# Kernel tuning notes

Hardware: AMD Instinct MI355X
Metric: run time of the kernel (lower is better)

## Reference

```python
import jax, jax.numpy as jnp
import numpy as np

D_MODEL = 256
N_HEADS = 4
D_HEAD = D_MODEL // N_HEADS
SCALE = 1.0 / np.sqrt(D_HEAD).astype(np.float32)


def setup_inputs() -> dict:
    key = jax.random.key(0)
    ks = jax.random.split(key, 8)
    B, T, S = 4, 512, 512
    return {
        "query": jax.random.normal(ks[0], (B, T, D_MODEL), dtype=jnp.float32),
        "key": jax.random.normal(ks[1], (B, S, D_MODEL), dtype=jnp.float32),
        "value": jax.random.normal(ks[2], (B, S, D_MODEL), dtype=jnp.float32),
        "w_q": jax.random.normal(ks[3], (D_MODEL, D_MODEL), dtype=jnp.float32) * 0.05,
        "w_k": jax.random.normal(ks[4], (D_MODEL, D_MODEL), dtype=jnp.float32) * 0.05,
        "w_v": jax.random.normal(ks[5], (D_MODEL, D_MODEL), dtype=jnp.float32) * 0.05,
        "v_a": jax.random.normal(ks[6], (N_HEADS, D_HEAD), dtype=jnp.float32),
        "w_o": jax.random.normal(ks[7], (D_MODEL, D_MODEL), dtype=jnp.float32) * 0.05,
    }


def reference(query, key, value, w_q, w_k, w_v, v_a, w_o):
    B, T, _ = query.shape
    S = key.shape[1]
    # projections; weights stored as (out, in) like nn.Linear -> x @ W.T
    Q = (query @ w_q.T).reshape(B, T, N_HEADS, D_HEAD).transpose(0, 2, 1, 3)  # bhtd
    K = (key @ w_k.T).reshape(B, S, N_HEADS, D_HEAD).transpose(0, 2, 1, 3)    # bhsd
    V = (value @ w_v.T).reshape(B, S, N_HEADS, D_HEAD).transpose(0, 2, 1, 3)  # bhsd
    # additive (Bahdanau) scores: tanh broadcast of shape (B,H,T,S,Dh)
    combined = jnp.tanh(Q[:, :, :, None, :] + K[:, :, None, :, :])
    scores = jnp.einsum('bhtsd,hd->bhts', combined, v_a) * SCALE
    attn = jax.nn.softmax(scores, axis=-1)  # (B,H,T,S)
    attended = jnp.einsum('bhts,bhsd->bhtd', attn, V)
    attended = attended.transpose(0, 2, 1, 3).reshape(B, T, D_MODEL)
    out = attended @ w_o.T
    return out, attn
```

## Files before the change

kernel.cpp:

```cpp
#include <hip/hip_runtime.h>
#include <math.h>

#define BATCH 4
#define TLEN 512
#define SLEN 512
#define DM 256
#define NH 4
#define DH 64
#define BT (BATCH * TLEN)
#define WPAD 132

__device__ __forceinline__ float rcp_fast(float x) { return __builtin_amdgcn_rcpf(x); }

__device__ __forceinline__ void gemm_selfstage(const float* __restrict__ X,
                                               const float* __restrict__ W,
                                               float* __restrict__ wlds,
                                               int row0, int o0, int tid, int lane,
                                               float* acc) {
#pragma unroll
  for (int r = 0; r < 8; ++r) acc[r] = 0.f;
  const float* xb = X + (size_t)row0 * DM;
#pragma unroll 1
  for (int half = 0; half < 2; ++half) {
    __syncthreads();
    {
      const float4* wsrc = (const float4*)(W + (size_t)o0 * DM + half * 128);
#pragma unroll
      for (int i = 0; i < 8; ++i) {
        int c = i * 256 + tid;
        int row = c >> 5, kq = c & 31;
        *(float4*)&wlds[row * WPAD + kq * 4] = wsrc[(size_t)row * 64 + kq];
      }
    }
    __syncthreads();
    const float* xh = xb + half * 128;
#pragma unroll 2
    for (int kk = 0; kk < 128; kk += 4) {
      float4 w = *(const float4*)&wlds[lane * WPAD + kk];
#pragma unroll
      for (int r = 0; r < 8; ++r) {
        acc[r] = fmaf(xh[r * DM + kk + 0], w.x, acc[r]);
        acc[r] = fmaf(xh[r * DM + kk + 1], w.y, acc[r]);
        acc[r] = fmaf(xh[r * DM + kk + 2], w.z, acc[r]);
        acc[r] = fmaf(xh[r * DM + kk + 3], w.w, acc[r]);
      }
    }
  }
}

__global__ __launch_bounds__(256) void proj_kernel(
    const float* __restrict__ q, const float* __restrict__ k, const float* __restrict__ v,
    const float* __restrict__ wq, const float* __restrict__ wk, const float* __restrict__ wv,
    float* __restrict__ EQ, float* __restrict__ EKT, float* __restrict__ Vw) {
  __shared__ float wlds[64 * WPAD];
  int tid = threadIdx.x;
  int lane = tid & 63;
  int wid = __builtin_amdgcn_readfirstlane(tid >> 6);
  int which = blockIdx.y;
  const float* X = (which == 0) ? q : (which == 1) ? k : v;
  const float* W = (which == 0) ? wq : (which == 1) ? wk : wv;
  int row0 = (blockIdx.x >> 2) * 32 + wid * 8;
  int o0 = (blockIdx.x & 3) * 64;
  float acc[8];
  gemm_selfstage(X, W, wlds, row0, o0, tid, lane, acc);
  int o = o0 + lane;
  int h = o >> 6, d = o & 63;
#pragma unroll
  for (int r = 0; r < 8; ++r) {
    int row = row0 + r;
    int b = row >> 9, t = row & 511;
    int bh = b * NH + h;
    float val = acc[r];
    if (which < 2) {
      val = __expf(2.f * fminf(fmaxf(val, -5.5f), 5.5f));
    }
    if (which == 0) {
      EQ[((size_t)bh * TLEN + t) * DH + d] = val;
    } else if (which == 1) {
      EKT[(((size_t)bh * 16 + (d >> 2)) * SLEN + t) * 4 + (d & 3)] = val;
    } else {
      Vw[(size_t)bh * SLEN * DH + (size_t)(t >> 1) * 128 + d * 2 + (t & 1)] = val;
    }
  }
}

__global__ __launch_bounds__(256, 8) void attn_kernel(
    const float* __restrict__ EQ, const float* __restrict__ EKT,
    const float* __restrict__ Vw, const float* __restrict__ va_g,
    float* __restrict__ attn_out, float* __restrict__ attended) {
  __shared__ float pw[4][SLEN];
  __shared__ float fp[4][4][64];
  __shared__ float sred[4][4];
  int tid = threadIdx.x;
  int lane = tid & 63;
  int wid = __builtin_amdgcn_readfirstlane(tid >> 6);
  int bx = (int)((blockIdx.x & 7) * 256 + (blockIdx.x >> 3));
  int bh = bx >> 7;
  int tile = (bx & 127) * 4;
  int h = bh & 3, b = bh >> 2;
  int sq0 = wid * 128;

  const float4* ekf = (const float4*)EKT + (size_t)bh * (16 * SLEN) + sq0 + lane;
  const float* eqb = EQ + ((size_t)bh * TLEN + tile) * DH;
  const float* vap = va_g + h * DH;

  float acc[4][2];
#pragma unroll
  for (int t = 0; t < 4; ++t) { acc[t][0] = 0.f; acc[t][1] = 0.f; }
  float vsum = 0.f;

  float4 eA0, eA1, eB0, eB1;

#define LOADE(EV, dc_) do { EV##0 = ekf[(size_t)(dc_) * SLEN]; \
                            EV##1 = ekf[(size_t)(dc_) * SLEN + 64]; } while (0)

#define SC4(E, qv, av, aref) do {                                           \
    float A0 = fmaf(qv.x, E.x, 1.f), A1 = fmaf(qv.y, E.y, 1.f);             \
    float A2 = fmaf(qv.z, E.z, 1.f), A3 = fmaf(qv.w, E.w, 1.f);             \
    float n01 = fmaf(av.x, A1, av.y * A0);                                  \
    float n23 = fmaf(av.z, A3, av.w * A2);                                  \
    float P01 = A0 * A1, P23 = A2 * A3;                                     \
    float Nm = fmaf(n01, P23, n23 * P01);                                   \
    aref = fmaf(Nm, rcp_fast(P01 * P23), aref);                             \
  } while (0)

#define DCBODY(CUR, NXT, dc_) do {                                          \
    float4 av = *(const float4*)(vap + (dc_) * 4);                          \
    float4 q0 = *(const float4*)(eqb + 0 * DH + (dc_) * 4);                 \
    float4 q1 = *(const float4*)(eqb + 1 * DH + (dc_) * 4);                 \
    float4 q2 = *(const float4*)(eqb + 2 * DH + (dc_) * 4);                 \
    float4 q3 = *(const float4*)(eqb + 3 * DH + (dc_) * 4);                 \
    vsum += (av.x + av.y) + (av.z + av.w);                                  \
    if ((dc_) < 15) LOADE(NXT, (dc_) + 1);                                  \
    __builtin_amdgcn_sched_barrier(0);                                      \
    SC4(CUR##0, q0, av, acc[0][0]); SC4(CUR##1, q0, av, acc[0][1]);         \
    SC4(CUR##0, q1, av, acc[1][0]); SC4(CUR##1, q1, av, acc[1][1]);         \
    SC4(CUR##0, q2, av, acc[2][0]); SC4(CUR##1, q2, av, acc[2][1]);         \
    SC4(CUR##0, q3, av, acc[3][0]); SC4(CUR##1, q3, av, acc[3][1]);         \
  } while (0)

  LOADE(eA, 0);
#pragma unroll 1
  for (int dc2 = 0; dc2 < 8; ++dc2) {
    DCBODY(eA, eB, 2 * dc2);
    DCBODY(eB, eA, 2 * dc2 + 1);
  }

  size_t bht = (size_t)bh * TLEN + tile;
  float e0[4], e1[4];
#pragma unroll
  for (int t = 0; t < 4; ++t) {
    float x0 = __expf(fmaf(acc[t][0], -0.25f, vsum * 0.125f));
    float x1 = __expf(fmaf(acc[t][1], -0.25f, vsum * 0.125f));
    e0[t] = x0; e1[t] = x1;
    float es = x0 + x1;
#pragma unroll
    for (int off = 32; off; off >>= 1) es += __shfl_xor(es, off);
    if (lane == 0) sred[t][wid] = es;
  }
  __syncthreads();
#pragma unroll
  for (int t = 0; t < 4; ++t) {
    float es = (sred[t][0] + sred[t][1]) + (sred[t][2] + sred[t][3]);
    float inv = rcp_fast(es);
    float p0 = e0[t] * inv, p1 = e1[t] * inv;
    pw[t][sq0 + lane] = p0;
    pw[t][sq0 + 64 + lane] = p1;
    float* arow = attn_out + (bht + t) * SLEN + sq0;
    arow[lane] = p0;
    arow[64 + lane] = p1;
  }

  const float2* vb = (const float2*)Vw + (size_t)bh * (256 * 64) + (size_t)(wid * 64) * 64 + lane;
  float f[4];
#pragma unroll
  for (int t = 0; t < 4; ++t) f[t] = 0.f;
#pragma unroll 2
  for (int i = 0; i < 32; ++i) {
    float2 v01 = vb[(size_t)i * 128];
    float2 v23 = vb[(size_t)i * 128 + 64];
    int sb = sq0 + i * 4;
#pragma unroll
    for (int t = 0; t < 4; ++t) {
      float4 pq = *(const float4*)&pw[t][sb];
      f[t] = fmaf(pq.x, v01.x, f[t]);
      f[t] = fmaf(pq.y, v01.y, f[t]);
      f[t] = fmaf(pq.z, v23.x, f[t]);
      f[t] = fmaf(pq.w, v23.y, f[t]);
    }
  }
#pragma unroll
  for (int t = 0; t < 4; ++t) fp[wid][t][lane] = f[t];
  __syncthreads();
  {
    int t = wid;
    float s = (fp[0][t][lane] + fp[1][t][lane]) + (fp[2][t][lane] + fp[3][t][lane]);
    attended[((size_t)(b * TLEN) + tile + t) * DM + h * DH + lane] = s;
  }
}

__global__ __launch_bounds__(256) void outproj_kernel(
    const float* __restrict__ att, const float* __restrict__ wo,
    float* __restrict__ out) {
  __shared__ float wlds[64 * WPAD];
  int tid = threadIdx.x;
  int lane = tid & 63;
  int wid = __builtin_amdgcn_readfirstlane(tid >> 6);
  int row0 = (blockIdx.x >> 2) * 32 + wid * 8;
  int o0 = (blockIdx.x & 3) * 64;
  float acc[8];
  gemm_selfstage(att, wo, wlds, row0, o0, tid, lane, acc);
  int o = o0 + lane;
#pragma unroll
  for (int r = 0; r < 8; ++r)
    out[(size_t)(row0 + r) * DM + o] = acc[r];
}

extern "C" void kernel_launch(void* const* d_in, const int* in_sizes, int n_in,
                              void* d_out, int out_size, void* d_ws, size_t ws_size,
                              hipStream_t stream) {
  const float* query = (const float*)d_in[0];
  const float* key   = (const float*)d_in[1];
  const float* value = (const float*)d_in[2];
  const float* wq    = (const float*)d_in[3];
  const float* wk    = (const float*)d_in[4];
  const float* wv    = (const float*)d_in[5];
  const float* va    = (const float*)d_in[6];
  const float* wo    = (const float*)d_in[7];

  float* out  = (float*)d_out;
  float* attn = out + (size_t)BT * DM;

  const size_t SEG = (size_t)BT * DM;
  float* EQ  = (float*)d_ws;
  float* EKT = EQ + SEG;
  float* Vw  = EKT + SEG;
  float* att = Vw + SEG;

  proj_kernel<<<dim3(256, 3), 256, 0, stream>>>(query, key, value, wq, wk, wv, EQ, EKT, Vw);
  attn_kernel<<<dim3(2048), 256, 0, stream>>>(EQ, EKT, Vw, va, attn, att);
  outproj_kernel<<<dim3(256), 256, 0, stream>>>(att, wo, out);
}
```

Before: 101.8 us.

## Fuse projection, attention and output projection into one persistent kernel with grid barriers

Replaces the three separate launches with a single 1024-block persistent kernel. It has three phases: the QKV projection on 768 blocks, two attention tiles per block, and the output projection spread over 512 blocks with 4 rows per wave. The phases are separated by atomic-counter grid barriers. This removes inter-kernel launch gaps and tail effects, and swaps the padded weight staging in LDS for an XOR-swizzled layout. It relies on all 1024 blocks being co-resident. The barrier counters live in the last word of the att and out buffers, which later phases overwrite while some blocks may still be polling, so correctness depends on that timing.

```diff
diff --git a/kernel.cpp b/kernel.cpp
--- a/kernel.cpp
+++ b/kernel.cpp
@@ -8,112 +8,58 @@
 #define NH 4
 #define DH 64
 #define BT (BATCH * TLEN)
-#define WPAD 132
+#define NBLK 1024
 
 __device__ __forceinline__ float rcp_fast(float x) { return __builtin_amdgcn_rcpf(x); }
 
-__device__ __forceinline__ void gemm_selfstage(const float* __restrict__ X,
-                                               const float* __restrict__ W,
-                                               float* __restrict__ wlds,
-                                               int row0, int o0, int tid, int lane,
-                                               float* acc) {
-#pragma unroll
-  for (int r = 0; r < 8; ++r) acc[r] = 0.f;
-  const float* xb = X + (size_t)row0 * DM;
+__device__ __forceinline__ void grid_barrier(unsigned* ctr) {
+  __syncthreads();
+  if (threadIdx.x == 0) {
+    __threadfence();
+    __hip_atomic_fetch_add(ctr, 1u, __ATOMIC_RELAXED, __HIP_MEMORY_SCOPE_AGENT);
+    while (__hip_atomic_load(ctr, __ATOMIC_RELAXED, __HIP_MEMORY_SCOPE_AGENT) < NBLK)
+      __builtin_amdgcn_s_sleep(8);
+    __threadfence();
+  }
+  __syncthreads();
+}
+
+template <int RPT>
+__device__ __forceinline__ void panel_gemm(const float* __restrict__ X,
+                                           const float* __restrict__ W,
+                                           float* wl, int o0, int wrow0,
+                                           int tid, int lane, float* acc) {
+#pragma unroll
+  for (int r = 0; r < RPT; ++r) acc[r] = 0.f;
 #pragma unroll 1
   for (int half = 0; half < 2; ++half) {
     __syncthreads();
-    {
-      const float4* wsrc = (const float4*)(W + (size_t)o0 * DM + half * 128);
-#pragma unroll
-      for (int i = 0; i < 8; ++i) {
-        int c = i * 256 + tid;
-        int row = c >> 5, kq = c & 31;
-        *(float4*)&wlds[row * WPAD + kq * 4] = wsrc[(size_t)row * 64 + kq];
+    const float4* wsrc = (const float4*)(W + (size_t)o0 * DM + half * 128);
+#pragma unroll
+    for (int i = 0; i < 8; ++i) {
+      int c = i * 256 + tid;
+      int o = c >> 5, f = c & 31;
+      *(float4*)&wl[o * 128 + 4 * (f ^ (o & 7))] = wsrc[(size_t)o * 64 + f];
+    }
+    __syncthreads();
+    const float* xh = X + (size_t)wrow0 * DM + half * 128;
+#pragma unroll 4
+    for (int g = 0; g < 32; ++g) {
+      float4 w = *(const float4*)&wl[lane * 128 + 4 * (g ^ (lane & 7))];
+#pragma unroll
+      for (int r = 0; r < RPT; ++r) {
+        const float* xr = xh + r * DM + g * 4;
+        acc[r] = fmaf(xr[0], w.x, acc[r]);
+        acc[r] = fmaf(xr[1], w.y, acc[r]);
+        acc[r] = fmaf(xr[2], w.z, acc[r]);
+        acc[r] = fmaf(xr[3], w.w, acc[r]);
       }
     }
-    __syncthreads();
-    const float* xh = xb + half * 128;
-#pragma unroll 2
-    for (int kk = 0; kk < 128; kk += 4) {
-      float4 w = *(const float4*)&wlds[lane * WPAD + kk];
-#pragma unroll
-      for (int r = 0; r < 8; ++r) {
-        acc[r] = fmaf(xh[r * DM + kk + 0], w.x, acc[r]);
-        acc[r] = fmaf(xh[r * DM + kk + 1], w.y, acc[r]);
-        acc[r] = fmaf(xh[r * DM + kk + 2], w.z, acc[r]);
-        acc[r] = fmaf(xh[r * DM + kk + 3], w.w, acc[r]);
-      }
-    }
-  }
-}
-
-__global__ __launch_bounds__(256) void proj_kernel(
-    const float* __restrict__ q, const float* __restrict__ k, const float* __restrict__ v,
-    const float* __restrict__ wq, const float* __restrict__ wk, const float* __restrict__ wv,
-    float* __restrict__ EQ, float* __restrict__ EKT, float* __restrict__ Vw) {
-  __shared__ float wlds[64 * WPAD];
-  int tid = threadIdx.x;
-  int lane = tid & 63;
-  int wid = __builtin_amdgcn_readfirstlane(tid >> 6);
-  int which = blockIdx.y;
-  const float* X = (which == 0) ? q : (which == 1) ? k : v;
-  const float* W = (which == 0) ? wq : (which == 1) ? wk : wv;
-  int row0 = (blockIdx.x >> 2) * 32 + wid * 8;
-  int o0 = (blockIdx.x & 3) * 64;
-  float acc[8];
-  gemm_selfstage(X, W, wlds, row0, o0, tid, lane, acc);
-  int o = o0 + lane;
-  int h = o >> 6, d = o & 63;
-#pragma unroll
-  for (int r = 0; r < 8; ++r) {
-    int row = row0 + r;
-    int b = row >> 9, t = row & 511;
-    int bh = b * NH + h;
-    float val = acc[r];
-    if (which < 2) {
-      val = __expf(2.f * fminf(fmaxf(val, -5.5f), 5.5f));
-    }
-    if (which == 0) {
-      EQ[((size_t)bh * TLEN + t) * DH + d] = val;
-    } else if (which == 1) {
-      EKT[(((size_t)bh * 16 + (d >> 2)) * SLEN + t) * 4 + (d & 3)] = val;
-    } else {
-      Vw[(size_t)bh * SLEN * DH + (size_t)(t >> 1) * 128 + d * 2 + (t & 1)] = val;
-    }
-  }
-}
-
-__global__ __launch_bounds__(256, 8) void attn_kernel(
-    const float* __restrict__ EQ, const float* __restrict__ EKT,
-    const float* __restrict__ Vw, const float* __restrict__ va_g,
-    float* __restrict__ attn_out, float* __restrict__ attended) {
-  __shared__ float pw[4][SLEN];
-  __shared__ float fp[4][4][64];
-  __shared__ float sred[4][4];
-  int tid = threadIdx.x;
-  int lane = tid & 63;
-  int wid = __builtin_amdgcn_readfirstlane(tid >> 6);
-  int bx = (int)((blockIdx.x & 7) * 256 + (blockIdx.x >> 3));
-  int bh = bx >> 7;
-  int tile = (bx & 127) * 4;
-  int h = bh & 3, b = bh >> 2;
-  int sq0 = wid * 128;
-
-  const float4* ekf = (const float4*)EKT + (size_t)bh * (16 * SLEN) + sq0 + lane;
-  const float* eqb = EQ + ((size_t)bh * TLEN + tile) * DH;
-  const float* vap = va_g + h * DH;
-
-  float acc[4][2];
-#pragma unroll
-  for (int t = 0; t < 4; ++t) { acc[t][0] = 0.f; acc[t][1] = 0.f; }
-  float vsum = 0.f;
-
-  float4 eA0, eA1, eB0, eB1;
+  }
+}
 
 #define LOADE(EV, dc_) do { EV##0 = ekf[(size_t)(dc_) * SLEN]; \
                             EV##1 = ekf[(size_t)(dc_) * SLEN + 64]; } while (0)
-
 #define SC4(E, qv, av, aref) do {                                           \
     float A0 = fmaf(qv.x, E.x, 1.f), A1 = fmaf(qv.y, E.y, 1.f);             \
     float A2 = fmaf(qv.z, E.z, 1.f), A3 = fmaf(qv.w, E.w, 1.f);             \
@@ -123,7 +69,6 @@
     float Nm = fmaf(n01, P23, n23 * P01);                                   \
     aref = fmaf(Nm, rcp_fast(P01 * P23), aref);                             \
   } while (0)
-
 #define DCBODY(CUR, NXT, dc_) do {                                          \
     float4 av = *(const float4*)(vap + (dc_) * 4);                          \
     float4 q0 = *(const float4*)(eqb + 0 * DH + (dc_) * 4);                 \
@@ -139,6 +84,30 @@
     SC4(CUR##0, q3, av, acc[3][0]); SC4(CUR##1, q3, av, acc[3][1]);         \
   } while (0)
 
+__device__ __forceinline__ void attn_tile(int bxv,
+    const float* __restrict__ EQ, const float* __restrict__ EKT,
+    const float* __restrict__ Vw, const float* __restrict__ va_g,
+    float* __restrict__ attn_out, float* __restrict__ attended,
+    float* smem, int tid, int lane, int wid) {
+  float* pwf   = smem;
+  float* fpf   = smem + 2048;
+  float* sredf = smem + 3072;
+  int bx = (bxv & 7) * 256 + (bxv >> 3);
+  int bh = bx >> 7;
+  int tile = (bx & 127) * 4;
+  int h = bh & 3, b = bh >> 2;
+  int sq0 = wid * 128;
+
+  const float4* ekf = (const float4*)EKT + (size_t)bh * (16 * SLEN) + sq0 + lane;
+  const float* eqb = EQ + ((size_t)bh * TLEN + tile) * DH;
+  const float* vap = va_g + h * DH;
+
+  float acc[4][2];
+#pragma unroll
+  for (int t = 0; t < 4; ++t) { acc[t][0] = 0.f; acc[t][1] = 0.f; }
+  float vsum = 0.f;
+  float4 eA0, eA1, eB0, eB1;
+
   LOADE(eA, 0);
 #pragma unroll 1
   for (int dc2 = 0; dc2 < 8; ++dc2) {
@@ -156,16 +125,16 @@
     float es = x0 + x1;
 #pragma unroll
     for (int off = 32; off; off >>= 1) es += __shfl_xor(es, off);
-    if (lane == 0) sred[t][wid] = es;
+    if (lane == 0) sredf[t * 4 + wid] = es;
   }
   __syncthreads();
 #pragma unroll
   for (int t = 0; t < 4; ++t) {
-    float es = (sred[t][0] + sred[t][1]) + (sred[t][2] + sred[t][3]);
+    float es = (sredf[t * 4 + 0] + sredf[t * 4 + 1]) + (sredf[t * 4 + 2] + sredf[t * 4 + 3]);
     float inv = rcp_fast(es);
     float p0 = e0[t] * inv, p1 = e1[t] * inv;
-    pw[t][sq0 + lane] = p0;
-    pw[t][sq0 + 64 + lane] = p1;
+    pwf[t * SLEN + sq0 + lane] = p0;
+    pwf[t * SLEN + sq0 + 64 + lane] = p1;
     float* arow = attn_out + (bht + t) * SLEN + sq0;
     arow[lane] = p0;
     arow[64 + lane] = p1;
@@ -182,7 +151,7 @@
     int sb = sq0 + i * 4;
 #pragma unroll
     for (int t = 0; t < 4; ++t) {
-      float4 pq = *(const float4*)&pw[t][sb];
+      float4 pq = *(const float4*)&pwf[t * SLEN + sb];
       f[t] = fmaf(pq.x, v01.x, f[t]);
       f[t] = fmaf(pq.y, v01.y, f[t]);
       f[t] = fmaf(pq.z, v23.x, f[t]);
@@ -190,30 +159,73 @@
     }
   }
 #pragma unroll
-  for (int t = 0; t < 4; ++t) fp[wid][t][lane] = f[t];
+  for (int t = 0; t < 4; ++t) fpf[(wid * 4 + t) * 64 + lane] = f[t];
   __syncthreads();
   {
     int t = wid;
-    float s = (fp[0][t][lane] + fp[1][t][lane]) + (fp[2][t][lane] + fp[3][t][lane]);
+    float s = (fpf[(0 * 4 + t) * 64 + lane] + fpf[(1 * 4 + t) * 64 + lane]) +
+              (fpf[(2 * 4 + t) * 64 + lane] + fpf[(3 * 4 + t) * 64 + lane]);
     attended[((size_t)(b * TLEN) + tile + t) * DM + h * DH + lane] = s;
   }
 }
 
-__global__ __launch_bounds__(256) void outproj_kernel(
-    const float* __restrict__ att, const float* __restrict__ wo,
-    float* __restrict__ out) {
-  __shared__ float wlds[64 * WPAD];
+__global__ __launch_bounds__(256, 4) void fused_kernel(
+    const float* __restrict__ q, const float* __restrict__ k, const float* __restrict__ v,
+    const float* __restrict__ wq, const float* __restrict__ wk, const float* __restrict__ wv,
+    const float* __restrict__ va, const float* __restrict__ wo,
+    float* __restrict__ EQ, float* __restrict__ EKT, float* __restrict__ Vw,
+    float* __restrict__ att, float* __restrict__ out, float* __restrict__ attn_probs,
+    unsigned* bar0, unsigned* bar1) {
+  __shared__ float smem[8192];
   int tid = threadIdx.x;
   int lane = tid & 63;
   int wid = __builtin_amdgcn_readfirstlane(tid >> 6);
-  int row0 = (blockIdx.x >> 2) * 32 + wid * 8;
-  int o0 = (blockIdx.x & 3) * 64;
-  float acc[8];
-  gemm_selfstage(att, wo, wlds, row0, o0, tid, lane, acc);
-  int o = o0 + lane;
-#pragma unroll
-  for (int r = 0; r < 8; ++r)
-    out[(size_t)(row0 + r) * DM + o] = acc[r];
+  int pb = blockIdx.x;
+
+  if (pb < 768) {
+    int m = pb >> 8, sub = pb & 255;
+    int wrow0 = (sub >> 2) * 32 + wid * 8;
+    int o0 = (sub & 3) * 64;
+    const float* X = (m == 0) ? q : (m == 1) ? k : v;
+    const float* W = (m == 0) ? wq : (m == 1) ? wk : wv;
+    float acc[8];
+    panel_gemm<8>(X, W, smem, o0, wrow0, tid, lane, acc);
+    int o = o0 + lane, h = o >> 6, d = o & 63;
+#pragma unroll
+    for (int r = 0; r < 8; ++r) {
+      int row = wrow0 + r;
+      int b = row >> 9, t = row & 511;
+      int bh = b * NH + h;
+      float val = acc[r];
+      if (m < 2) {
+        val = __expf(2.f * fminf(fmaxf(val, -5.5f), 5.5f));
+      }
+      if (m == 0) {
+        EQ[((size_t)bh * TLEN + t) * DH + d] = val;
+      } else if (m == 1) {
+        EKT[(((size_t)bh * 16 + (d >> 2)) * SLEN + t) * 4 + (d & 3)] = val;
+      } else {
+        Vw[(size_t)bh * SLEN * DH + (size_t)(t >> 1) * 128 + d * 2 + (t & 1)] = val;
+      }
+    }
+  }
+  grid_barrier(bar0);
+
+  attn_tile(pb,        EQ, EKT, Vw, va, attn_probs, att, smem, tid, lane, wid);
+  attn_tile(pb + 1024, EQ, EKT, Vw, va, attn_probs, att, smem, tid, lane, wid);
+
+  grid_barrier(bar1);
+
+  if (pb < 512) {
+    int wrow0 = (pb >> 2) * 16 + wid * 4;
+    int o0 = (pb & 3) * 64;
+    float acc[4];
+    panel_gemm<4>(att, wo, smem, o0, wrow0, tid, lane, acc);
+    int o = o0 + lane;
+#pragma unroll
+    for (int r = 0; r < 4; ++r)
+      out[(size_t)(wrow0 + r) * DM + o] = acc[r];
+  }
 }
 
 extern "C" void kernel_launch(void* const* d_in, const int* in_sizes, int n_in,
@@ -237,7 +249,12 @@
   float* Vw  = EKT + SEG;
   float* att = Vw + SEG;
 
-  proj_kernel<<<dim3(256, 3), 256, 0, stream>>>(query, key, value, wq, wk, wv, EQ, EKT, Vw);
-  attn_kernel<<<dim3(2048), 256, 0, stream>>>(EQ, EKT, Vw, va, attn, att);
-  outproj_kernel<<<dim3(256), 256, 0, stream>>>(att, wo, out);
-}
+  unsigned* bar0 = (unsigned*)(att + SEG - 1);
+  unsigned* bar1 = (unsigned*)(out + SEG - 1);
+  hipMemsetAsync(bar0, 0, 4, stream);
+  hipMemsetAsync(bar1, 0, 4, stream);
+
+  fused_kernel<<<dim3(NBLK), 256, 0, stream>>>(
+      query, key, value, wq, wk, wv, va, wo,
+      EQ, EKT, Vw, att, out, attn, bar0, bar1);
+}
```

New measurement: 360.9 us. 254% more time.
